# Kernel optimization log

Measured on AMD Instinct MI355X. Metric: run time of the kernel, lower is better.

## Reference

```python
import jax, jax.numpy as jnp
import numpy as np

VOCAB, EMB, HID, NTAG, SEQ = 50000, 256, 512, 20, 8192
H = HID // 2  # per-direction hidden size


def _lstm_dir(x, Wih, Whh, bih, bhh, reverse):
    # x: [S, E]; PyTorch gate order i, f, g, o
    h0 = jnp.zeros((H,), x.dtype)
    c0 = jnp.zeros((H,), x.dtype)
    b = bih + bhh
    xg = x @ Wih.T + b  # [S, 4H] precompute input projection

    def step(carry, xt):
        h, c = carry
        gates = xt + h @ Whh.T
        i, f, g, o = jnp.split(gates, 4)
        i = jax.nn.sigmoid(i)
        f = jax.nn.sigmoid(f)
        g = jnp.tanh(g)
        o = jax.nn.sigmoid(o)
        c = f * c + i * g
        h = o * jnp.tanh(c)
        return (h, c), h

    _, hs = jax.lax.scan(step, (h0, c0), xg, reverse=reverse)
    return hs  # [S, H]


def _viterbi(emissions, start_trans, end_trans, trans):
    # emissions [S, T]; torchcrf-style Viterbi decode
    score0 = start_trans + emissions[0]

    def fwd(score, em):
        tot = score[:, None] + trans          # [T_from, T_to]
        bp = jnp.argmax(tot, axis=0)          # best previous tag per next tag
        score = jnp.max(tot, axis=0) + em
        return score, bp

    final, bps = jax.lax.scan(fwd, score0, emissions[1:])
    final = final + end_trans
    last = jnp.argmax(final).astype(jnp.int32)

    def back(tag, bp):
        prev = bp[tag].astype(jnp.int32)
        return prev, prev

    _, prevs = jax.lax.scan(back, last, bps, reverse=True)
    return jnp.concatenate([prevs, last[None]])  # [S]


def setup_inputs() -> dict:
    key = jax.random.key(0)
    ks = jax.random.split(key, 16)
    s = 0.1
    inp = {
        "sentence": jax.random.randint(ks[0], (SEQ,), 0, VOCAB, dtype=jnp.int64)
                    if jax.config.read("jax_enable_x64") else
                    jax.random.randint(ks[0], (SEQ,), 0, VOCAB, dtype=jnp.int32),
        "embed": jax.random.normal(ks[1], (VOCAB, EMB), jnp.float32),
        "Wih_f": jax.random.normal(ks[2], (4 * H, EMB), jnp.float32) * s,
        "Whh_f": jax.random.normal(ks[3], (4 * H, H), jnp.float32) * s,
        "bih_f": jax.random.normal(ks[4], (4 * H,), jnp.float32) * s,
        "bhh_f": jax.random.normal(ks[5], (4 * H,), jnp.float32) * s,
        "Wih_b": jax.random.normal(ks[6], (4 * H, EMB), jnp.float32) * s,
        "Whh_b": jax.random.normal(ks[7], (4 * H, H), jnp.float32) * s,
        "bih_b": jax.random.normal(ks[8], (4 * H,), jnp.float32) * s,
        "bhh_b": jax.random.normal(ks[9], (4 * H,), jnp.float32) * s,
        "Wout": jax.random.normal(ks[10], (NTAG, HID), jnp.float32) * s,
        "bout": jax.random.normal(ks[11], (NTAG,), jnp.float32) * s,
        "start_trans": jax.random.normal(ks[12], (NTAG,), jnp.float32) * s,
        "end_trans": jax.random.normal(ks[13], (NTAG,), jnp.float32) * s,
        "trans": jax.random.normal(ks[14], (NTAG, NTAG), jnp.float32) * s,
    }
    return inp


def reference(sentence, embed, Wih_f, Whh_f, bih_f, bhh_f,
              Wih_b, Whh_b, bih_b, bhh_b, Wout, bout,
              start_trans, end_trans, trans):
    x = embed[sentence]                                  # [S, E]
    h_f = _lstm_dir(x, Wih_f, Whh_f, bih_f, bhh_f, reverse=False)
    h_b = _lstm_dir(x, Wih_b, Whh_b, bih_b, bhh_b, reverse=True)
    lstm_out = jnp.concatenate([h_f, h_b], axis=-1)      # [S, HID]; dropout is eval-mode identity
    emissions = lstm_out @ Wout.T + bout                 # [S, T]
    path = _viterbi(emissions, start_trans, end_trans, trans)
    return path
```

## Files before the change

### kernel.cpp

```cpp
#include <hip/hip_runtime.h>
#include <hip/hip_bf16.h>


#define S    8192
#define E    256
#define Hh   256
#define G    1024
#define NT   20
#define NB   4
#define NCHUNK 128
#define CLEN   64
#define SENT 0x7FC0DEADu

__global__ __launch_bounds__(256) void sentinel_fill(unsigned int* __restrict__ lo_u)
{
    size_t base = (size_t)blockIdx.x * 1024 + threadIdx.x;
    #pragma unroll
    for (int i = 0; i < 4; ++i)
        __hip_atomic_store(&lo_u[base + (size_t)i * 256], SENT,
                           __ATOMIC_RELAXED, __HIP_MEMORY_SCOPE_AGENT);
}

__global__ __launch_bounds__(1024, 4) void xg_project(
    const int* __restrict__ sent, const float* __restrict__ embed,
    const float* __restrict__ Wih_f, const float* __restrict__ bih_f, const float* __restrict__ bhh_f,
    const float* __restrict__ Wih_b, const float* __restrict__ bih_b, const float* __restrict__ bhh_b,
    float* __restrict__ xg)
{
    const int tb  = blockIdx.x;
    const int rb  = blockIdx.y;
    const int dir = blockIdx.z;
    const int tid = threadIdx.x;
    const int q   = tid >> 8;
    const int idx = tid & 255;
    const int r   = rb * 256 + idx;
    const float* Wih = dir ? Wih_b : Wih_f;

    __shared__ __align__(16) float4 xs4[32 * 64];
    __shared__ float psum[1024];

    const int t0 = tb * 32;
    #pragma unroll
    for (int i = 0; i < 2; ++i) {
        int qq  = i * 1024 + tid;
        int row = qq >> 6;
        int c4  = qq & 63;
        int widx = sent[t0 + row];
        xs4[qq] = *(const float4*)(embed + (size_t)widx * E + (size_t)c4 * 4);
    }

    float w[64];
    #pragma unroll
    for (int k = 0; k < 64; k += 4) {
        float4 v = *(const float4*)(Wih + (size_t)r * E + q * 64 + k);
        w[k] = v.x; w[k+1] = v.y; w[k+2] = v.z; w[k+3] = v.w;
    }
    float bias = 0.f;
    if (tid < 256) bias = dir ? (bih_b[r] + bhh_b[r]) : (bih_f[r] + bhh_f[r]);
    __syncthreads();

    const float* xs = (const float*)xs4 + q * 64;
    float* outb = xg + ((size_t)dir * S + t0) * G + r;
    for (int tt = 0; tt < 32; ++tt) {
        float a0 = 0.f, a1 = 0.f, a2 = 0.f, a3 = 0.f;
        #pragma unroll
        for (int k = 0; k < 64; k += 4) {
            float4 h4 = *(const float4*)(xs + tt * E + k);
            a0 = fmaf(w[k],   h4.x, a0);
            a1 = fmaf(w[k+1], h4.y, a1);
            a2 = fmaf(w[k+2], h4.z, a2);
            a3 = fmaf(w[k+3], h4.w, a3);
        }
        psum[tid] = (a0 + a1) + (a2 + a3);
        __syncthreads();
        if (tid < 256)
            outb[(size_t)tt * G] = bias +
                ((psum[idx] + psum[idx + 256]) + (psum[idx + 512] + psum[idx + 768]));
        __syncthreads();
    }
}

__global__ __launch_bounds__(1024, 4) void lstm_scan_mc(
    const float* __restrict__ xg,
    const float* __restrict__ Whh_f,
    const float* __restrict__ Whh_b,
    float* __restrict__ out)
{
    const int b    = blockIdx.x;
    const int dir  = blockIdx.y;
    const int tid  = threadIdx.x;
    const int q    = tid >> 8;
    const int idx  = tid & 255;
    const int gate = idx >> 6;
    const int hloc = idx & 63;
    const int hidx = b * 64 + hloc;
    const int row  = gate * Hh + hidx;
    const float* W   = dir ? Whh_b : Whh_f;
    const float* xgd = xg + (size_t)dir * S * G;

    float w[64];
    #pragma unroll
    for (int k = 0; k < 64; k += 4) {
        float4 v = *(const float4*)(W + (size_t)row * Hh + q * 64 + k);
        w[k] = v.x; w[k+1] = v.y; w[k+2] = v.z; w[k+3] = v.w;
    }

    __shared__ __align__(16) float h_lds[Hh];
    __shared__ float psum[1024];
    __shared__ float gates_lds[256];
    if (tid < Hh) h_lds[tid] = 0.f;
    float c = 0.f;

    const int t0 = dir ? (S - 1) : 0;
    const int dt = dir ? -1 : 1;
    float xg_cur = (tid < 256) ? xgd[(size_t)t0 * G + row] : 0.f;
    __syncthreads();

    for (int s = 0; s < S; ++s) {
        const int t = t0 + dt * s;
        float xg_next = 0.f;
        if (tid < 256 && s + 1 < S) xg_next = xgd[(size_t)(t + dt) * G + row];

        const float* hh = (const float*)h_lds + q * 64;
        float a0 = 0.f, a1 = 0.f, a2 = 0.f, a3 = 0.f;
        #pragma unroll
        for (int k = 0; k < 64; k += 4) {
            float4 h4 = *(const float4*)(hh + k);
            a0 = fmaf(w[k],   h4.x, a0);
            a1 = fmaf(w[k+1], h4.y, a1);
            a2 = fmaf(w[k+2], h4.z, a2);
            a3 = fmaf(w[k+3], h4.w, a3);
        }
        psum[tid] = (a0 + a1) + (a2 + a3);
        __syncthreads();

        if (tid < 256) {
            float acc = xg_cur +
                ((psum[idx] + psum[idx + 256]) + (psum[idx + 512] + psum[idx + 768]));
            float a = (gate == 2) ? tanhf(acc) : 1.f / (1.f + expf(-acc));
            gates_lds[idx] = a;
        }
        __syncthreads();

        if (tid < 64) {
            float iv = gates_lds[hloc];
            float fv = gates_lds[64 + hloc];
            float gv = gates_lds[128 + hloc];
            float ov = gates_lds[192 + hloc];
            c = fv * c + iv * gv;
            float h = ov * tanhf(c);
            __hip_atomic_store(out + (size_t)t * 512 + dir * Hh + hidx, h,
                               __ATOMIC_RELAXED, __HIP_MEMORY_SCOPE_AGENT);
            h_lds[hidx] = h;
        }
        if (s + 1 < S && tid < Hh && (tid >> 6) != b) {
            const unsigned int* srcp =
                (const unsigned int*)(out + (size_t)t * 512 + dir * Hh + tid);
            unsigned int v;
            do {
                v = __hip_atomic_load(srcp, __ATOMIC_RELAXED,
                                      __HIP_MEMORY_SCOPE_AGENT);
            } while (v == SENT);
            h_lds[tid] = __uint_as_float(v);
        }
        __syncthreads();
        xg_cur = xg_next;
    }
}

__global__ __launch_bounds__(256) void emissions_kernel(
    const float* __restrict__ lo,
    const float* __restrict__ Wout,
    const float* __restrict__ bout,
    float* __restrict__ em)
{
    int gid = blockIdx.x * blockDim.x + threadIdx.x;
    if (gid >= S * NT) return;
    int t = gid / NT;
    int j = gid - t * NT;
    const float* x = lo + (size_t)t * 512;
    const float* w = Wout + (size_t)j * 512;
    float a0 = 0.f, a1 = 0.f, a2 = 0.f, a3 = 0.f;
    #pragma unroll 8
    for (int k = 0; k < 512; k += 4) {
        float4 xv = *(const float4*)(x + k);
        float4 wv = *(const float4*)(w + k);
        a0 = fmaf(xv.x, wv.x, a0);
        a1 = fmaf(xv.y, wv.y, a1);
        a2 = fmaf(xv.z, wv.z, a2);
        a3 = fmaf(xv.w, wv.w, a3);
    }
    em[gid] = bout[j] + ((a0 + a1) + (a2 + a3));
}

__global__ __launch_bounds__(64) void viterbi_fwd(
    const float* __restrict__ em,
    const float* __restrict__ start_trans,
    const float* __restrict__ end_trans,
    const float* __restrict__ trans,
    unsigned char* __restrict__ bp,
    int* __restrict__ last_out)
{
    const int lane = threadIdx.x;
    const int g    = lane / 20;
    const int j    = lane - g * 20;
    const int i0   = g * 7;

    float tc[7];
    #pragma unroll
    for (int u = 0; u < 7; ++u) {
        int i = i0 + u;
        tc[u] = (g < 3 && i < 20) ? trans[i * NT + j] : -3.0e38f;
    }

    const int jj = (g < 3) ? j : 0;
    float snew  = start_trans[jj] + em[jj];
    if (g == 0) bp[j] = (unsigned char)j;
    float e_cur = em[NT + jj];

    for (int t = 1; t < S; ++t) {
        float s_sub[7];
        #pragma unroll
        for (int u = 0; u < 7; ++u)
            s_sub[u] = __shfl(snew, i0 + u);
        float e_nxt = (t + 1 < S) ? em[(size_t)(t + 1) * NT + jj] : 0.f;

        float bv = s_sub[0] + tc[0];
        int   bi = i0;
        #pragma unroll
        for (int u = 1; u < 7; ++u) {
            float v = s_sub[u] + tc[u];
            if (v > bv) { bv = v; bi = i0 + u; }
        }
        float v0 = __shfl(bv, jj), v1 = __shfl(bv, jj + 20), v2 = __shfl(bv, jj + 40);
        int   c0 = __shfl(bi, jj), c1 = __shfl(bi, jj + 20), c2 = __shfl(bi, jj + 40);
        float best = v0; int bidx = c0;
        if (v1 > best) { best = v1; bidx = c1; }
        if (v2 > best) { best = v2; bidx = c2; }
        snew = best + e_cur;
        if (g == 0) bp[(size_t)t * NT + j] = (unsigned char)bidx;
        e_cur = e_nxt;
    }

    float bv = __shfl(snew, 0) + end_trans[0];
    int   bi = 0;
    #pragma unroll 1
    for (int i = 1; i < 20; ++i) {
        float v = __shfl(snew, i) + end_trans[i];
        if (v > bv) { bv = v; bi = i; }
    }
    if (lane == 0) *last_out = bi;
}

__global__ __launch_bounds__(64) void bt_maps(
    const unsigned char* __restrict__ bp, unsigned char* __restrict__ maps)
{
    __shared__ unsigned char lbp[CLEN * NT];
    const int c = blockIdx.x, tid = threadIdx.x;
    const unsigned* src = (const unsigned*)(bp + (size_t)c * CLEN * NT);
    unsigned* dst = (unsigned*)lbp;
    for (int q = tid; q < CLEN * NT / 4; q += 64) dst[q] = src[q];
    __syncthreads();
    if (tid < NT) {
        int x = tid;
        for (int t = CLEN - 1; t >= 0; --t) x = lbp[t * NT + x];
        maps[c * NT + tid] = (unsigned char)x;
    }
}

__global__ __launch_bounds__(64) void bt_boundary(
    const unsigned char* __restrict__ maps, const int* __restrict__ last_out,
    int* __restrict__ btags)
{
    __shared__ unsigned char m[NCHUNK * NT];
    const int tid = threadIdx.x;
    for (int q = tid; q < NCHUNK * NT; q += 64) m[q] = maps[q];
    __syncthreads();
    if (tid == 0) {
        int x = *last_out;
        btags[NCHUNK - 1] = x;
        for (int c = NCHUNK - 1; c >= 1; --c) {
            x = m[c * NT + x];
            btags[c - 1] = x;
        }
    }
}

__global__ __launch_bounds__(64) void bt_emit(
    const unsigned char* __restrict__ bp, const int* __restrict__ btags,
    int* __restrict__ path)
{
    __shared__ unsigned char lbp[CLEN * NT];
    const int c = blockIdx.x, tid = threadIdx.x;
    const unsigned* src = (const unsigned*)(bp + (size_t)c * CLEN * NT);
    unsigned* dst = (unsigned*)lbp;
    for (int q = tid; q < CLEN * NT / 4; q += 64) dst[q] = src[q];
    __syncthreads();
    if (tid == 0) {
        int x = btags[c];
        path[c * CLEN + CLEN - 1] = x;
        for (int t = CLEN - 1; t >= 1; --t) {
            x = lbp[t * NT + x];
            path[c * CLEN + t - 1] = x;
        }
    }
}

extern "C" void kernel_launch(void* const* d_in, const int* in_sizes, int n_in,
                              void* d_out, int out_size, void* d_ws, size_t ws_size,
                              hipStream_t stream) {
    const int*   sent   = (const int*)  d_in[0];
    const float* embed  = (const float*)d_in[1];
    const float* Wih_f  = (const float*)d_in[2];
    const float* Whh_f  = (const float*)d_in[3];
    const float* bih_f  = (const float*)d_in[4];
    const float* bhh_f  = (const float*)d_in[5];
    const float* Wih_b  = (const float*)d_in[6];
    const float* Whh_b  = (const float*)d_in[7];
    const float* bih_b  = (const float*)d_in[8];
    const float* bhh_b  = (const float*)d_in[9];
    const float* Wout   = (const float*)d_in[10];
    const float* bout   = (const float*)d_in[11];
    const float* start_trans = (const float*)d_in[12];
    const float* end_trans   = (const float*)d_in[13];
    const float* trans       = (const float*)d_in[14];
    int* path = (int*)d_out;

    char* ws = (char*)d_ws;
    size_t off = 0;
    float* xg = (float*)(ws + off); off += (size_t)2 * S * G * 4;
    float* lo = (float*)(ws + off); off += (size_t)S * 512 * 4;
    float* em = (float*)(ws + off); off += (size_t)S * NT * 4;
    unsigned char* bp   = (unsigned char*)(ws + off); off += (size_t)S * NT;
    unsigned char* maps = (unsigned char*)(ws + off); off += 4096;
    int* btags = (int*)(ws + off); off += 1024;
    int* lastp = (int*)(ws + off); off += 256;

    sentinel_fill<<<dim3(4096), 256, 0, stream>>>((unsigned int*)lo);
    xg_project<<<dim3(S / 32, 4, 2), 1024, 0, stream>>>(
        sent, embed, Wih_f, bih_f, bhh_f, Wih_b, bih_b, bhh_b, xg);
    lstm_scan_mc<<<dim3(NB, 2), 1024, 0, stream>>>(xg, Whh_f, Whh_b, lo);
    emissions_kernel<<<dim3((S * NT + 255) / 256), 256, 0, stream>>>(lo, Wout, bout, em);
    viterbi_fwd<<<dim3(1), 64, 0, stream>>>(em, start_trans, end_trans, trans, bp, lastp);
    bt_maps<<<dim3(NCHUNK), 64, 0, stream>>>(bp, maps);
    bt_boundary<<<dim3(1), 64, 0, stream>>>(maps, lastp, btags);
    bt_emit<<<dim3(NCHUNK), 64, 0, stream>>>(bp, btags, path);
}
```

Measured before the change: 15.61 ms.

## Use per-consumer double-buffered mailboxes with asm polling for LSTM hidden-state exchange

Hidden-state exchange between the four blocks of each direction now goes through small per-producer/per-consumer mailboxes, double-buffered by step parity. Each consumer resets its slot to a sentinel after reading, so the full-output sentinel fill kernel is gone. Dedicated poll warps spin with an unrolled inline-asm ring of uncached loads. Gates are interleaved per hidden unit and combined with warp shuffles, which removes one LDS round-trip and one barrier per step. The xg prefetch is also deepened to two steps. The goal is lower per-step cross-block latency, at the cost of complex asm. There is also a fallback path that polls the output buffer against a 0xAAAAAAAA poison value, so correctness there depends on how the workspace is initialised.

Result: slower. 17.52 ms (+12.2%).

```diff
diff --git a/kernel.cpp b/kernel.cpp
--- a/kernel.cpp
+++ b/kernel.cpp
@@ -10,15 +10,13 @@
 #define NB   4
 #define NCHUNK 128
 #define CLEN   64
-#define SENT 0x7FC0DEADu
-
-__global__ __launch_bounds__(256) void sentinel_fill(unsigned int* __restrict__ lo_u)
-{
-    size_t base = (size_t)blockIdx.x * 1024 + threadIdx.x;
-    #pragma unroll
-    for (int i = 0; i < 4; ++i)
-        __hip_atomic_store(&lo_u[base + (size_t)i * 256], SENT,
-                           __ATOMIC_RELAXED, __HIP_MEMORY_SCOPE_AGENT);
+#define SENTU 0x7FC0DEADu
+#define POISON 0xAAAAAAAAu
+
+__global__ __launch_bounds__(256) void priv_init(unsigned* __restrict__ p)
+{
+    int i = blockIdx.x * 256 + threadIdx.x;
+    if (i < 4096) p[i] = SENTU;
 }
 
 __global__ __launch_bounds__(1024, 4) void xg_project(
@@ -80,21 +78,21 @@
     }
 }
 
-__global__ __launch_bounds__(1024, 4) void lstm_scan_mc(
+__global__ __launch_bounds__(1024, 4) void lstm_scan4(
     const float* __restrict__ xg,
     const float* __restrict__ Whh_f,
     const float* __restrict__ Whh_b,
-    float* __restrict__ out)
-{
-    const int b    = blockIdx.x;
-    const int dir  = blockIdx.y;
-    const int tid  = threadIdx.x;
+    float* __restrict__ out,
+    float* __restrict__ priv)
+{
+    const int b   = blockIdx.x;
+    const int dir = blockIdx.y;
+    const int tid = threadIdx.x;
     const int q    = tid >> 8;
     const int idx  = tid & 255;
-    const int gate = idx >> 6;
-    const int hloc = idx & 63;
-    const int hidx = b * 64 + hloc;
-    const int row  = gate * Hh + hidx;
+    const int gate = idx & 3;
+    const int hloc = idx >> 2;
+    const int row  = gate * Hh + b * 64 + hloc;
     const float* W   = dir ? Whh_b : Whh_f;
     const float* xgd = xg + (size_t)dir * S * G;
 
@@ -107,19 +105,30 @@
 
     __shared__ __align__(16) float h_lds[Hh];
     __shared__ float psum[1024];
-    __shared__ float gates_lds[256];
     if (tid < Hh) h_lds[tid] = 0.f;
     float c = 0.f;
 
+    const bool isPoll = (tid >= 256 && tid < 448);
+    const int pl   = tid - 256;
+    const int pi   = pl >> 6;
+    const int word = pl & 63;
+    const int pb   = pi + (pi >= b);
+    const int lane = tid & 63;
+
     const int t0 = dir ? (S - 1) : 0;
     const int dt = dir ? -1 : 1;
-    float xg_cur = (tid < 256) ? xgd[(size_t)t0 * G + row] : 0.f;
+    float xg_c = 0.f, xg_n1 = 0.f;
+    if (tid < 256) {
+        xg_c  = xgd[(size_t)t0 * G + row];
+        xg_n1 = xgd[(size_t)(t0 + dt) * G + row];
+    }
+    unsigned g0 = 0, g1 = 0, g2 = 0, g3 = 0;
     __syncthreads();
 
     for (int s = 0; s < S; ++s) {
         const int t = t0 + dt * s;
-        float xg_next = 0.f;
-        if (tid < 256 && s + 1 < S) xg_next = xgd[(size_t)(t + dt) * G + row];
+        float xg_n2 = 0.f;
+        if (tid < 256 && s + 2 < S) xg_n2 = xgd[(size_t)(t + 2 * dt) * G + row];
 
         const float* hh = (const float*)h_lds + q * 64;
         float a0 = 0.f, a1 = 0.f, a2 = 0.f, a3 = 0.f;
@@ -135,37 +144,107 @@
         __syncthreads();
 
         if (tid < 256) {
-            float acc = xg_cur +
+            float acc = xg_c +
                 ((psum[idx] + psum[idx + 256]) + (psum[idx + 512] + psum[idx + 768]));
             float a = (gate == 2) ? tanhf(acc) : 1.f / (1.f + expf(-acc));
-            gates_lds[idx] = a;
+            float fv = __shfl_down(a, 1);
+            float gv = __shfl_down(a, 2);
+            float ov = __shfl_down(a, 3);
+            if (gate == 0) {
+                c = fv * c + a * gv;
+                float h = ov * tanhf(c);
+                const int par = s & 1;
+                #pragma unroll
+                for (int ci = 0; ci < 3; ++ci) {
+                    int cons = ci + (ci >= b);
+                    __hip_atomic_store(
+                        &priv[(((dir * 4 + cons) * 4 + b) * 2 + par) * 64 + hloc], h,
+                        __ATOMIC_RELAXED, __HIP_MEMORY_SCOPE_AGENT);
+                }
+                __hip_atomic_store(&out[(size_t)t * 512 + dir * Hh + b * 64 + hloc],
+                                   h, __ATOMIC_RELAXED, __HIP_MEMORY_SCOPE_AGENT);
+                h_lds[b * 64 + hloc] = h;
+            }
+        } else if (isPoll && s + 1 < S) {
+            const float* sp =
+                &priv[(((dir * 4 + b) * 4 + pb) * 2 + (s & 1)) * 64 + word];
+            unsigned res = 0, bud = 300;
+            unsigned long long dn = 0, rem;
+            asm volatile(
+                "global_load_dword %[g0], %[a], off sc0 sc1\n\t"
+                "s_waitcnt vmcnt(0)\n\t"
+                "v_cmp_ne_u32 vcc, 0x7fc0dead, %[g0]\n\t"
+                "v_cndmask_b32 %[res], %[res], %[g0], vcc\n\t"
+                "s_or_b64 %[dn], %[dn], vcc\n\t"
+                "s_andn2_b64 %[rem], exec, %[dn]\n\t"
+                "s_cbranch_scc0 RED%=\n\t"
+                "global_load_dword %[g0], %[a], off sc0 sc1\n\t"
+                "s_sleep 2\n\t"
+                "global_load_dword %[g1], %[a], off sc0 sc1\n\t"
+                "s_sleep 2\n\t"
+                "global_load_dword %[g2], %[a], off sc0 sc1\n\t"
+                "s_sleep 2\n\t"
+                "global_load_dword %[g3], %[a], off sc0 sc1\n\t"
+                "RING%=:\n\t"
+                "s_waitcnt vmcnt(3)\n\t"
+                "v_cmp_ne_u32 vcc, 0x7fc0dead, %[g0]\n\t"
+                "s_andn2_b64 vcc, vcc, %[dn]\n\t"
+                "v_cndmask_b32 %[res], %[res], %[g0], vcc\n\t"
+                "s_or_b64 %[dn], %[dn], vcc\n\t"
+                "s_andn2_b64 %[rem], exec, %[dn]\n\t"
+                "s_cbranch_scc0 RED%=\n\t"
+                "global_load_dword %[g0], %[a], off sc0 sc1\n\t"
+                "s_waitcnt vmcnt(3)\n\t"
+                "v_cmp_ne_u32 vcc, 0x7fc0dead, %[g1]\n\t"
+                "s_andn2_b64 vcc, vcc, %[dn]\n\t"
+                "v_cndmask_b32 %[res], %[res], %[g1], vcc\n\t"
+                "s_or_b64 %[dn], %[dn], vcc\n\t"
+                "s_andn2_b64 %[rem], exec, %[dn]\n\t"
+                "s_cbranch_scc0 RED%=\n\t"
+                "global_load_dword %[g1], %[a], off sc0 sc1\n\t"
+                "s_waitcnt vmcnt(3)\n\t"
+                "v_cmp_ne_u32 vcc, 0x7fc0dead, %[g2]\n\t"
+                "s_andn2_b64 vcc, vcc, %[dn]\n\t"
+                "v_cndmask_b32 %[res], %[res], %[g2], vcc\n\t"
+                "s_or_b64 %[dn], %[dn], vcc\n\t"
+                "s_andn2_b64 %[rem], exec, %[dn]\n\t"
+                "s_cbranch_scc0 RED%=\n\t"
+                "global_load_dword %[g2], %[a], off sc0 sc1\n\t"
+                "s_waitcnt vmcnt(3)\n\t"
+                "v_cmp_ne_u32 vcc, 0x7fc0dead, %[g3]\n\t"
+                "s_andn2_b64 vcc, vcc, %[dn]\n\t"
+                "v_cndmask_b32 %[res], %[res], %[g3], vcc\n\t"
+                "s_or_b64 %[dn], %[dn], vcc\n\t"
+                "s_andn2_b64 %[rem], exec, %[dn]\n\t"
+                "s_cbranch_scc0 RED%=\n\t"
+                "global_load_dword %[g3], %[a], off sc0 sc1\n\t"
+                "s_sub_u32 %[bud], %[bud], 1\n\t"
+                "s_cmp_lg_u32 %[bud], 0\n\t"
+                "s_cbranch_scc1 RING%=\n\t"
+                "RED%=:\n\t"
+                : [g0]"+v"(g0), [g1]"+v"(g1), [g2]"+v"(g2), [g3]"+v"(g3),
+                  [res]"+v"(res), [dn]"+s"(dn), [bud]"+s"(bud), [rem]"=s"(rem)
+                : [a]"v"(sp)
+                : "vcc", "memory");
+            if (!((dn >> lane) & 1)) {
+                const unsigned* op = (const unsigned*)
+                    (out + (size_t)t * 512 + dir * Hh + pb * 64 + word);
+                unsigned v;
+                do {
+                    v = __hip_atomic_load(op, __ATOMIC_RELAXED,
+                                          __HIP_MEMORY_SCOPE_AGENT);
+                } while (v == POISON);
+                res = v;
+            }
+            h_lds[pb * 64 + word] = __uint_as_float(res);
+            __hip_atomic_store((unsigned*)sp, SENTU,
+                               __ATOMIC_RELAXED, __HIP_MEMORY_SCOPE_AGENT);
         }
         __syncthreads();
-
-        if (tid < 64) {
-            float iv = gates_lds[hloc];
-            float fv = gates_lds[64 + hloc];
-            float gv = gates_lds[128 + hloc];
-            float ov = gates_lds[192 + hloc];
-            c = fv * c + iv * gv;
-            float h = ov * tanhf(c);
-            __hip_atomic_store(out + (size_t)t * 512 + dir * Hh + hidx, h,
-                               __ATOMIC_RELAXED, __HIP_MEMORY_SCOPE_AGENT);
-            h_lds[hidx] = h;
-        }
-        if (s + 1 < S && tid < Hh && (tid >> 6) != b) {
-            const unsigned int* srcp =
-                (const unsigned int*)(out + (size_t)t * 512 + dir * Hh + tid);
-            unsigned int v;
-            do {
-                v = __hip_atomic_load(srcp, __ATOMIC_RELAXED,
-                                      __HIP_MEMORY_SCOPE_AGENT);
-            } while (v == SENT);
-            h_lds[tid] = __uint_as_float(v);
-        }
-        __syncthreads();
-        xg_cur = xg_next;
-    }
+        xg_c = xg_n1; xg_n1 = xg_n2;
+    }
+    asm volatile("" :: "v"(g0), "v"(g1), "v"(g2), "v"(g3));
+    asm volatile("s_waitcnt vmcnt(0)" ::: "memory");
 }
 
 __global__ __launch_bounds__(256) void emissions_kernel(
@@ -335,11 +414,13 @@
     unsigned char* maps = (unsigned char*)(ws + off); off += 4096;
     int* btags = (int*)(ws + off); off += 1024;
     int* lastp = (int*)(ws + off); off += 256;
-
-    sentinel_fill<<<dim3(4096), 256, 0, stream>>>((unsigned int*)lo);
+    off = (off + 255) & ~(size_t)255;
+    float* priv = (float*)(ws + off); off += 4096 * 4;
+
+    priv_init<<<dim3(16), 256, 0, stream>>>((unsigned*)priv);
     xg_project<<<dim3(S / 32, 4, 2), 1024, 0, stream>>>(
         sent, embed, Wih_f, bih_f, bhh_f, Wih_b, bih_b, bhh_b, xg);
-    lstm_scan_mc<<<dim3(NB, 2), 1024, 0, stream>>>(xg, Whh_f, Whh_b, lo);
+    lstm_scan4<<<dim3(NB, 2), 1024, 0, stream>>>(xg, Whh_f, Whh_b, lo, priv);
     emissions_kernel<<<dim3((S * NT + 255) / 256), 256, 0, stream>>>(lo, Wout, bout, em);
     viterbi_fwd<<<dim3(1), 64, 0, stream>>>(em, start_trans, end_trans, trans, bp, lastp);
     bt_maps<<<dim3(NCHUNK), 64, 0, stream>>>(bp, maps);
```
